# Kernel optimization log

Hardware: AMD Instinct MI355X
Metric: run time of the kernel (lower is better)

## Reference

```python
import jax, jax.numpy as jnp
import numpy as np

S, B, T = 512, 128, 256

def setup_inputs() -> dict:
    key = jax.random.key(0)
    k1, k2, k3 = jax.random.split(key, 3)
    feats = jax.random.normal(k1, (S, B, T), dtype=jnp.float32)
    tags = jax.random.randint(k2, (S, B), 0, T, dtype=jnp.int64)
    mask = jnp.ones((S, B), dtype=jnp.int32)
    start_transitions = jnp.zeros((T,), dtype=jnp.float32)
    end_transitions = jnp.zeros((T,), dtype=jnp.float32)
    transitions = jax.random.normal(k3, (T, T), dtype=jnp.float32)
    return {"feats": feats, "tags": tags, "mask": mask,
            "start_transitions": start_transitions,
            "end_transitions": end_transitions,
            "transitions": transitions}

def _crf_loss(feats, tags, mask, start_transitions, end_transitions, transitions):
    # feats: [S, B, T]; tags, mask: [S, B]
    batch = tags.shape[1]
    mask_b = mask.astype(bool)
    mask_f = mask.astype(feats.dtype)

    # ---- forward (log-partition) via scan over time ----
    score0 = start_transitions + feats[0]  # [B, T]

    def step(score, xs):
        feat, m = xs  # feat: [B, T], m: [B] bool
        # [B, T_prev, T_next]
        nxt = jax.nn.logsumexp(score[:, :, None] + transitions[None, :, :] + feat[:, None, :], axis=1)
        score = jnp.where(m[:, None], nxt, score)
        return score, None

    score, _ = jax.lax.scan(step, score0, (feats[1:], mask_b[1:]))
    forward_score = jax.nn.logsumexp(score + end_transitions, axis=1)  # [B]

    # ---- gold path score, fully vectorized ----
    emit = jnp.take_along_axis(feats, tags[:, :, None], axis=2)[..., 0]  # [S, B]
    trans = transitions[tags[:-1], tags[1:]]  # [S-1, B]
    gold = start_transitions[tags[0]] + emit[0]
    gold = gold + jnp.sum((emit[1:] + trans) * mask_f[1:], axis=0)
    seq_ends = jnp.sum(mask, axis=0).astype(jnp.int32) - 1  # [B]
    last_tags = tags[seq_ends, jnp.arange(batch)]
    gold = gold + end_transitions[last_tags]

    return forward_score - gold  # [B]

def reference(feats, tags, mask, start_transitions, end_transitions, transitions):
    return _crf_loss(feats, tags, mask, start_transitions, end_transitions, transitions)
```

## Files before the change

### kernel.cpp

```cpp
#include <hip/hip_runtime.h>
#include <math.h>

#define S 512
#define B 128
#define T 256
#define NTH 256
#define LOG2E 1.44269504f
#define LN2 0.69314718f

typedef _Float16 h2 __attribute__((ext_vector_type(2)));

#if __has_builtin(__builtin_amdgcn_fdot2)
#define FDOT2(a, b, c) __builtin_amdgcn_fdot2((a), (b), (c), false)
#else
#define FDOT2(a, b, c) fmaf((float)(a)[0], (float)(b)[0], fmaf((float)(a)[1], (float)(b)[1], (c)))
#endif

#if __has_builtin(__builtin_amdgcn_exp2f)
#define EXP2(x) __builtin_amdgcn_exp2f(x)
#else
#define EXP2(x) exp2f(x)
#endif
#if __has_builtin(__builtin_amdgcn_logf)
#define LOG2F(x) __builtin_amdgcn_logf(x)
#else
#define LOG2F(x) __log2f(x)
#endif

#define AS1 __attribute__((address_space(1)))
#define AS3 __attribute__((address_space(3)))

#define BAR() do { asm volatile("s_waitcnt lgkmcnt(0)" ::: "memory"); __builtin_amdgcn_s_barrier(); } while (0)

__device__ __forceinline__ float mul2n(float x, int n) {
    return x * __builtin_bit_cast(float, (n + 127) << 23);
}

template<int CTRL, int RM>
__device__ __forceinline__ float dppmax(float x) {
    int xi = __builtin_bit_cast(int, x);
    int yi = __builtin_amdgcn_update_dpp(xi, xi, CTRL, RM, 0xf, false);
    return fmaxf(x, __builtin_bit_cast(float, yi));
}
__device__ __forceinline__ float wave_max64(float x) {
    x = dppmax<0x111, 0xf>(x);
    x = dppmax<0x112, 0xf>(x);
    x = dppmax<0x114, 0xf>(x);
    x = dppmax<0x118, 0xf>(x);
    x = dppmax<0x142, 0xa>(x);
    x = dppmax<0x143, 0xc>(x);
    return __builtin_bit_cast(float, __builtin_amdgcn_readlane(__builtin_bit_cast(int, x), 63));
}

__global__ __launch_bounds__(NTH, 1) void crf_fwd(
    const float* __restrict__ feats,
    const int*   __restrict__ tags,
    const int*   __restrict__ mask,
    const float* __restrict__ start_t,
    const float* __restrict__ end_t,
    const float* __restrict__ trans,
    float*       __restrict__ out)
{
    const int b    = blockIdx.x;
    const int j    = threadIdx.x;
    const int lane = j & 63;
    const int w    = j >> 6;

    __shared__ __attribute__((aligned(16))) _Float16 qbuf[2][T];
    __shared__ float ftile[8][T];
    __shared__ int   msk[S];
    __shared__ __attribute__((aligned(16))) float redq[2][4];
    __shared__ float redF[4], redS[4], redg[4], redm[4], redi[4];

    #pragma unroll
    for (int tn = 1; tn <= 4; ++tn) {
        const float* src = feats + ((size_t)tn * B + b) * T + j;
        __builtin_amdgcn_global_load_lds((const AS1 void*)src,
                                         (AS3 void*)&ftile[tn & 7][j], 4, 0, 0);
    }

    const float endj = end_t[j];
    const float sc0  = start_t[j] + feats[(size_t)b * T + j];
    msk[j]     = mask[j * B + b];
    msk[j + T] = mask[(j + T) * B + b];

    float gterm = 0.f, mcnt = 0.f;
    #pragma unroll
    for (int c = 0; c < 2; ++c) {
        const int t  = j + c * T;
        const int tg = tags[t * B + b];
        const int m  = mask[t * B + b];
        const float emit = feats[((size_t)t * B + b) * T + tg];
        mcnt += (float)m;
        if (t == 0) gterm += start_t[tg] + emit;
        else        gterm += m ? (emit + trans[tags[(t - 1) * B + b] * T + tg]) : 0.f;
    }
    #pragma unroll
    for (int o = 32; o > 0; o >>= 1) {
        gterm += __shfl_down(gterm, o, 64);
        mcnt  += __shfl_down(mcnt, o, 64);
    }
    if (lane == 0) { redg[w] = gterm; redm[w] = mcnt; }

    h2 E2[128];
    {
        const float* tc = trans + j;
        #pragma unroll
        for (int p = 0; p < 128; ++p) {
            const float e0 = EXP2(LOG2E * tc[(size_t)(2 * p) * T]);
            const float e1 = EXP2(LOG2E * tc[(size_t)(2 * p + 1) * T]);
            h2 v; v[0] = (_Float16)e0; v[1] = (_Float16)e1;
            E2[p] = v;
        }
    }

    {
        const float mx = wave_max64(sc0);
        if (lane == 0) redi[w] = mx;
    }
    __syncthreads();

    float gold = 0.f;
    if (j == 0) {
        const float g  = redg[0] + redg[1] + redg[2] + redg[3];
        const float mc = redm[0] + redm[1] + redm[2] + redm[3];
        gold = g + end_t[tags[((int)mc - 1) * B + b]];
    }

    const float gmax0 = fmaxf(fmaxf(redi[0], redi[1]), fmaxf(redi[2], redi[3]));
    int A = (int)ceilf(gmax0 * LOG2E) + 10;
    float q = EXP2(fmaf(sc0, LOG2E, (float)(-A)));
    qbuf[0][j] = (_Float16)q;
    {
        const float mq = wave_max64(q);
        if (lane == 0) redq[0][w] = mq;
    }
    float Fnext = EXP2(ftile[1][j] * LOG2E);
    __syncthreads();

    for (int t = 1; t < S; ++t) {
        const int cur = (t - 1) & 1;
        const float Fcur = Fnext;

        const float4 rq = *(const float4*)&redq[cur][0];
        const int2 qp   = *(const int2*)&qbuf[cur][4 * lane];
        const int mskt  = msk[t];

        if (t + 4 < S) {
            const float* src = feats + ((size_t)(t + 4) * B + b) * T + j;
            __builtin_amdgcn_global_load_lds((const AS1 void*)src,
                                             (AS3 void*)&ftile[(t + 4) & 7][j], 4, 0, 0);
            asm volatile("s_waitcnt vmcnt(3)" ::: "memory");
        } else if (t == S - 4) { asm volatile("s_waitcnt vmcnt(2)" ::: "memory"); }
        else if   (t == S - 3) { asm volatile("s_waitcnt vmcnt(1)" ::: "memory"); }
        else if   (t == S - 2) { asm volatile("s_waitcnt vmcnt(0)" ::: "memory"); }
        const float ftn = (t < S - 1) ? ftile[(t + 1) & 7][j] : 0.f;

        float a0 = 0.f, a1 = 0.f, a2 = 0.f, a3 = 0.f;
        int pr = __builtin_amdgcn_readlane(qp.x, 0);
        #pragma unroll
        for (int p = 0; p < 128; ++p) {
            const int prn = (p < 127)
                ? __builtin_amdgcn_readlane((p & 1) ? qp.x : qp.y, (p + 1) >> 1)
                : 0;
            const h2 pv = __builtin_bit_cast(h2, pr);
            if ((p & 3) == 0)      a0 = FDOT2(E2[p], pv, a0);
            else if ((p & 3) == 1) a1 = FDOT2(E2[p], pv, a1);
            else if ((p & 3) == 2) a2 = FDOT2(E2[p], pv, a2);
            else                   a3 = FDOT2(E2[p], pv, a3);
            pr = prn;
        }
        const float s = (a0 + a1) + (a2 + a3);

        const float gm = fmaxf(fmaxf(rq.x, rq.y), fmaxf(rq.z, rq.w));
        const int k = ((__builtin_bit_cast(int, gm) >> 23) & 0xff) - 117;
        const float s2k = __builtin_bit_cast(float, (127 - k) << 23);
        const float qn = s * (Fcur * s2k);
        const float qf = mul2n(q, -k);
        q = mskt ? qn : qf;
        A += k;
        qbuf[t & 1][j] = (_Float16)q;
        Fnext = EXP2(ftn * LOG2E);
        {
            const float mq = wave_max64(q);
            if (lane == 0) redq[t & 1][w] = mq;
        }
        BAR();
    }

    const float u2 = LOG2F(q) + (float)A + endj * LOG2E;
    {
        const float mw = wave_max64(u2);
        if (lane == 0) redF[w] = mw;
    }
    BAR();
    {
        const float gmax = fmaxf(fmaxf(redF[0], redF[1]), fmaxf(redF[2], redF[3]));
        float e = EXP2(u2 - gmax);
        #pragma unroll
        for (int o = 32; o > 0; o >>= 1) e += __shfl_xor(e, o, 64);
        if (lane == 0) redS[w] = e;
        BAR();
        if (j == 0) {
            const float ssum = redS[0] + redS[1] + redS[2] + redS[3];
            out[b] = (gmax + LOG2F(ssum)) * LN2 - gold;
        }
    }
}

extern "C" void kernel_launch(void* const* d_in, const int* in_sizes, int n_in,
                              void* d_out, int out_size, void* d_ws, size_t ws_size,
                              hipStream_t stream) {
    const float* feats  = (const float*)d_in[0];
    const int*   tags   = (const int*)d_in[1];
    const int*   mask   = (const int*)d_in[2];
    const float* startt = (const float*)d_in[3];
    const float* endt   = (const float*)d_in[4];
    const float* transt = (const float*)d_in[5];
    float* out = (float*)d_out;
    crf_fwd<<<dim3(B), dim3(NTH), 0, stream>>>(feats, tags, mask, startt, endt, transt, out);
}
```

Measured before the change: 401.8 us.

## Split CRF recurrence by previous-state per wave, combine partials through LDS

Each wave now owns the 64 previous states whose probabilities it already holds in registers. It computes partial dot products for all 256 next states, four per lane, using readlane broadcasts of its own q values, which are paired through a DPP quad shuffle. The four wave partials are written to a double-buffered LDS array and summed after the single per-step barrier. This removes the f16 q broadcast buffer in LDS and its load at the top of each step. In exchange, each step writes and reads four floats per thread of partial sums, and the transition matrix is loaded with float4 vectors in a new register layout.

```diff
diff --git a/kernel.cpp b/kernel.cpp
--- a/kernel.cpp
+++ b/kernel.cpp
@@ -50,6 +50,11 @@
     x = dppmax<0x142, 0xa>(x);
     x = dppmax<0x143, 0xc>(x);
     return __builtin_bit_cast(float, __builtin_amdgcn_readlane(__builtin_bit_cast(int, x), 63));
+}
+__device__ __forceinline__ float quad_next(float x) {
+    int xi = __builtin_bit_cast(int, x);
+    int yi = __builtin_amdgcn_update_dpp(xi, xi, 0xF5, 0xf, 0xf, false);
+    return __builtin_bit_cast(float, yi);
 }
 
 __global__ __launch_bounds__(NTH, 1) void crf_fwd(
@@ -66,7 +71,7 @@
     const int lane = j & 63;
     const int w    = j >> 6;
 
-    __shared__ __attribute__((aligned(16))) _Float16 qbuf[2][T];
+    __shared__ __attribute__((aligned(16))) float part[2][4][T];
     __shared__ float ftile[8][T];
     __shared__ int   msk[S];
     __shared__ __attribute__((aligned(16))) float redq[2][4];
@@ -102,15 +107,20 @@
     }
     if (lane == 0) { redg[w] = gterm; redm[w] = mcnt; }
 
-    h2 E2[128];
-    {
-        const float* tc = trans + j;
+    h2 E2[32][4];
+    {
+        const float* tp = trans + (size_t)(64 * w) * T + 4 * lane;
         #pragma unroll
-        for (int p = 0; p < 128; ++p) {
-            const float e0 = EXP2(LOG2E * tc[(size_t)(2 * p) * T]);
-            const float e1 = EXP2(LOG2E * tc[(size_t)(2 * p + 1) * T]);
-            h2 v; v[0] = (_Float16)e0; v[1] = (_Float16)e1;
-            E2[p] = v;
+        for (int ip = 0; ip < 32; ++ip) {
+            const float4 ra = *(const float4*)(tp + (size_t)(2 * ip) * T);
+            const float4 rb = *(const float4*)(tp + (size_t)(2 * ip + 1) * T);
+            #pragma unroll
+            for (int c = 0; c < 4; ++c) {
+                const float e0 = EXP2(LOG2E * (c == 0 ? ra.x : c == 1 ? ra.y : c == 2 ? ra.z : ra.w));
+                const float e1 = EXP2(LOG2E * (c == 0 ? rb.x : c == 1 ? rb.y : c == 2 ? rb.z : rb.w));
+                h2 v; v[0] = (_Float16)e0; v[1] = (_Float16)e1;
+                E2[ip][c] = v;
+            }
         }
     }
 
@@ -130,7 +140,12 @@
     const float gmax0 = fmaxf(fmaxf(redi[0], redi[1]), fmaxf(redi[2], redi[3]));
     int A = (int)ceilf(gmax0 * LOG2E) + 10;
     float q = EXP2(fmaf(sc0, LOG2E, (float)(-A)));
-    qbuf[0][j] = (_Float16)q;
+    int pki;
+    {
+        const float qnb = quad_next(q);
+        h2 v; v[0] = (_Float16)q; v[1] = (_Float16)qnb;
+        pki = __builtin_bit_cast(int, v);
+    }
     {
         const float mq = wave_max64(q);
         if (lane == 0) redq[0][w] = mq;
@@ -139,14 +154,26 @@
     __syncthreads();
 
     for (int t = 1; t < S; ++t) {
-        const int cur = (t - 1) & 1;
+        const int cur = (t - 1) & 1, nxt = t & 1;
         const float Fcur = Fnext;
 
-        const float4 rq = *(const float4*)&redq[cur][0];
-        const int2 qp   = *(const int2*)&qbuf[cur][4 * lane];
-        const int mskt  = msk[t];
-
-        if (t + 4 < S) {
+        float ax = 0.f, ay = 0.f, az = 0.f, aw = 0.f;
+        int pr0 = __builtin_amdgcn_readlane(pki, 0);
+        #pragma unroll
+        for (int ip = 0; ip < 32; ++ip) {
+            const int pr1 = (ip < 31) ? __builtin_amdgcn_readlane(pki, 2 * ip + 2) : 0;
+            const h2 pp = __builtin_bit_cast(h2, pr0);
+            ax = FDOT2(E2[ip][0], pp, ax);
+            ay = FDOT2(E2[ip][1], pp, ay);
+            az = FDOT2(E2[ip][2], pp, az);
+            aw = FDOT2(E2[ip][3], pp, aw);
+            pr0 = pr1;
+        }
+        {
+            float4 acc; acc.x = ax; acc.y = ay; acc.z = az; acc.w = aw;
+            *(float4*)&part[nxt][w][4 * lane] = acc;
+        }
+        if (t <= S - 5) {
             const float* src = feats + ((size_t)(t + 4) * B + b) * T + j;
             __builtin_amdgcn_global_load_lds((const AS1 void*)src,
                                              (AS3 void*)&ftile[(t + 4) & 7][j], 4, 0, 0);
@@ -154,39 +181,37 @@
         } else if (t == S - 4) { asm volatile("s_waitcnt vmcnt(2)" ::: "memory"); }
         else if   (t == S - 3) { asm volatile("s_waitcnt vmcnt(1)" ::: "memory"); }
         else if   (t == S - 2) { asm volatile("s_waitcnt vmcnt(0)" ::: "memory"); }
+        BAR();
+
+        const float4 rq = *(const float4*)&redq[cur][0];
+        const float s0 = part[nxt][0][j];
+        const float s1 = part[nxt][1][j];
+        const float s2 = part[nxt][2][j];
+        const float s3 = part[nxt][3][j];
         const float ftn = (t < S - 1) ? ftile[(t + 1) & 7][j] : 0.f;
-
-        float a0 = 0.f, a1 = 0.f, a2 = 0.f, a3 = 0.f;
-        int pr = __builtin_amdgcn_readlane(qp.x, 0);
-        #pragma unroll
-        for (int p = 0; p < 128; ++p) {
-            const int prn = (p < 127)
-                ? __builtin_amdgcn_readlane((p & 1) ? qp.x : qp.y, (p + 1) >> 1)
-                : 0;
-            const h2 pv = __builtin_bit_cast(h2, pr);
-            if ((p & 3) == 0)      a0 = FDOT2(E2[p], pv, a0);
-            else if ((p & 3) == 1) a1 = FDOT2(E2[p], pv, a1);
-            else if ((p & 3) == 2) a2 = FDOT2(E2[p], pv, a2);
-            else                   a3 = FDOT2(E2[p], pv, a3);
-            pr = prn;
-        }
-        const float s = (a0 + a1) + (a2 + a3);
-
+        const int mskt = msk[t];
         const float gm = fmaxf(fmaxf(rq.x, rq.y), fmaxf(rq.z, rq.w));
         const int k = ((__builtin_bit_cast(int, gm) >> 23) & 0xff) - 117;
         const float s2k = __builtin_bit_cast(float, (127 - k) << 23);
-        const float qn = s * (Fcur * s2k);
+        const float Fs = Fcur * s2k;
+        const float cb = (s0 + s1) + (s2 + s3);
+        const float qn = cb * Fs;
         const float qf = mul2n(q, -k);
         q = mskt ? qn : qf;
         A += k;
-        qbuf[t & 1][j] = (_Float16)q;
-        Fnext = EXP2(ftn * LOG2E);
+        {
+            const float qnb = quad_next(q);
+            h2 v; v[0] = (_Float16)q; v[1] = (_Float16)qnb;
+            pki = __builtin_bit_cast(int, v);
+        }
         {
             const float mq = wave_max64(q);
-            if (lane == 0) redq[t & 1][w] = mq;
-        }
-        BAR();
-    }
+            if (lane == 0) redq[nxt][w] = mq;
+        }
+        Fnext = EXP2(ftn * LOG2E);
+    }
+
+    BAR();
 
     const float u2 = LOG2F(q) + (float)A + endj * LOG2E;
     {
```

Result: faster. 352.1 us (-12.4%).
